# Kernel tuning notes

Hardware: AMD Instinct MI355X
Metric: run time of the kernel (lower is better)

Reference implementation:

```python
import jax, jax.numpy as jnp
import numpy as np

B, D, H, L, M = 32768, 768, 1024, 256, 32  # batch, input_dim, hidden, latent, context_memory_size
LN_EPS = 1e-5


def _ln(x, g, b):
    mu = jnp.mean(x, axis=-1, keepdims=True)
    var = jnp.mean(jnp.square(x - mu), axis=-1, keepdims=True)
    return (x - mu) * jax.lax.rsqrt(var + LN_EPS) * g + b


def _lrelu(x):
    return jnp.where(x >= 0, x, 0.2 * x)


def setup_inputs() -> dict:
    key = jax.random.key(0)
    ks = jax.random.split(key, 32)
    w = lambda k, shp: jax.random.normal(k, shp, jnp.float32) * (0.7 / np.sqrt(shp[-1]))
    return {
        "x": jax.random.normal(ks[0], (B, D), jnp.float32),
        "eps": jax.random.normal(ks[1], (B, L), jnp.float32),
        # encoder
        "enc_w1": w(ks[2], (H, D)), "enc_b1": jnp.zeros((H,), jnp.float32),
        "ln1_g": jnp.ones((H,), jnp.float32), "ln1_b": jnp.zeros((H,), jnp.float32),
        "enc_w2": w(ks[3], (H, H)), "enc_b2": jnp.zeros((H,), jnp.float32),
        "ln2_g": jnp.ones((H,), jnp.float32), "ln2_b": jnp.zeros((H,), jnp.float32),
        "mu_w": w(ks[4], (L, H)), "mu_b": jnp.zeros((L,), jnp.float32),
        "lv_w": w(ks[5], (L, H)), "lv_b": jnp.zeros((L,), jnp.float32),
        # decoder
        "di_w": w(ks[6], (H, L)), "di_b": jnp.zeros((H,), jnp.float32),
        "dec_w1": w(ks[7], (H, H)), "dec_b1": jnp.zeros((H,), jnp.float32),
        "dln1_g": jnp.ones((H,), jnp.float32), "dln1_b": jnp.zeros((H,), jnp.float32),
        "dec_w2": w(ks[8], (2 * H, H)), "dec_b2": jnp.zeros((2 * H,), jnp.float32),
        "dln2_g": jnp.ones((2 * H,), jnp.float32), "dln2_b": jnp.zeros((2 * H,), jnp.float32),
        "dec_w3": w(ks[9], (D, 2 * H)), "dec_b3": jnp.zeros((D,), jnp.float32),
        "ctx_mem": jax.random.normal(ks[10], (M, L), jnp.float32),
    }


def reference(x, eps, enc_w1, enc_b1, ln1_g, ln1_b, enc_w2, enc_b2, ln2_g, ln2_b,
              mu_w, mu_b, lv_w, lv_b, di_w, di_b, dec_w1, dec_b1, dln1_g, dln1_b,
              dec_w2, dec_b2, dln2_g, dln2_b, dec_w3, dec_b3, ctx_mem):
    # encode (Dropout is identity in eval mode)
    h = _lrelu(_ln(x @ enc_w1.T + enc_b1, ln1_g, ln1_b))
    h = _lrelu(_ln(h @ enc_w2.T + enc_b2, ln2_g, ln2_b))
    mu = h @ mu_w.T + mu_b
    logvar = h @ lv_w.T + lv_b
    # reparameterize
    z = mu + eps * jnp.exp(0.5 * logvar)
    # enhanced decode: context-memory attention
    attn = jax.nn.softmax(z @ ctx_mem.T, axis=-1)        # [B, M]
    z_enh = z + 0.1 * (attn @ ctx_mem)                   # [B, L]
    d = _lrelu(z_enh @ di_w.T + di_b)
    d = _lrelu(_ln(d @ dec_w1.T + dec_b1, dln1_g, dln1_b))
    d = _lrelu(_ln(d @ dec_w2.T + dec_b2, dln2_g, dln2_b))  # [B, 2H]
    reconstructed = d @ dec_w3.T + dec_b3                # [B, D]
    return reconstructed, mu, logvar
```

## Files before the change

### kernel.cpp

```cpp
#include <hip/hip_runtime.h>
#include <stdint.h>

#define DEV __device__ __forceinline__

typedef short bf16x8 __attribute__((ext_vector_type(8)));
typedef float f32x4 __attribute__((ext_vector_type(4)));

DEV ushort f2bf(float x) {
  uint32_t u = __builtin_bit_cast(uint32_t, x);
  return (ushort)((u + 0x7fffu + ((u >> 16) & 1u)) >> 16);
}
DEV float bf2f(ushort h) { return __builtin_bit_cast(float, (uint32_t)h << 16); }

DEV void gload_lds16(const void* g, void* l) {
  __builtin_amdgcn_global_load_lds((const __attribute__((address_space(1))) uint32_t*)g,
                                   (__attribute__((address_space(3))) uint32_t*)l, 16, 0, 0);
}

DEV bf16x8 ldv(const void* p) { return *(const bf16x8*)p; }

#define BARRIER __builtin_amdgcn_s_barrier()
#define SCHED0 __builtin_amdgcn_sched_barrier(0)
#define PRIO1 __builtin_amdgcn_s_setprio(1)
#define PRIO0 __builtin_amdgcn_s_setprio(0)
#define LGKM0                                        \
  do {                                               \
    asm volatile("s_waitcnt lgkmcnt(0)" ::: "memory"); \
    SCHED0;                                          \
  } while (0)

#define MFMA16(MH, NH, F, Bq)                                                   \
  _Pragma("unroll") for (int mi = 0; mi < 4; ++mi) {                            \
    _Pragma("unroll") for (int ni = 0; ni < 2; ++ni) {                          \
      acc[(MH)*4 + mi][(NH)*2 + ni] = __builtin_amdgcn_mfma_f32_16x16x32_bf16(  \
          F[mi][0], Bq[ni][0], acc[(MH)*4 + mi][(NH)*2 + ni], 0, 0, 0);         \
      acc[(MH)*4 + mi][(NH)*2 + ni] = __builtin_amdgcn_mfma_f32_16x16x32_bf16(  \
          F[mi][1], Bq[ni][1], acc[(MH)*4 + mi][(NH)*2 + ni], 0, 0, 0);         \
    }                                                                           \
  }

template <int EPI>
__global__ __launch_bounds__(512, 2) void g256(
    const ushort* __restrict__ A, int lda, const ushort* __restrict__ W, int ldb,
    void* __restrict__ Cv, long ldc, const float* __restrict__ bias,
    const float* __restrict__ bias2, long splitStride, int K) {
  __shared__ ushort As[2][256 * 64];
  __shared__ ushort Bs[2][256 * 64];
  const int t = threadIdx.x;
  const int l = t & 63;
  const int w = t >> 6;
  const int wm = w >> 2, wn = w & 3;

  const int nwg = gridDim.x * gridDim.y;
  int bid = blockIdx.y * gridDim.x + blockIdx.x;
  const int cpx = nwg >> 3;
  bid = (bid & 7) * cpx + (bid >> 3);
  const int bx = bid % gridDim.x;
  const int by = bid / gridDim.x;
  const long rowBase = (long)by << 8;
  const int colBase = bx << 8;

  const int srow = l >> 3;
  const int scol = ((l & 7) ^ srow) << 3;
  const ushort* aB = A + (size_t)(rowBase + srow) * lda + scol;
  const ushort* bB = W + (size_t)(colBase + srow) * ldb + scol;
  const int aC0 = wm * 16 + wn * 2;
  const int aC2 = aC0 + 8;
  const int bC0 = (wn >> 1) * 16 + (wm * 2 + (wn & 1)) * 4;

  const int fro = l & 15;
  const int o0 = (((l >> 4) << 4)) ^ ((l & 7) << 4);
  const int o1 = (64 + ((l >> 4) << 4)) ^ ((l & 7) << 4);

#define STG_A(KT1, CH) \
  gload_lds16(aB + (size_t)((CH) << 3) * lda + ((size_t)(KT1) << 6), \
              (char*)As[(KT1) & 1] + ((CH) << 10))
#define STG_B(KT1, CH) \
  gload_lds16(bB + (size_t)((CH) << 3) * ldb + ((size_t)(KT1) << 6), \
              (char*)Bs[(KT1) & 1] + ((CH) << 10))

  STG_A(0, aC0); STG_A(0, aC0 + 1);
  STG_B(0, bC0); STG_B(0, bC0 + 1); STG_B(0, bC0 + 2); STG_B(0, bC0 + 3);
  STG_A(0, aC2); STG_A(0, aC2 + 1);
  asm volatile("s_waitcnt vmcnt(2)" ::: "memory");
  BARRIER;

  const int nk = K >> 6;
  f32x4 acc[8][4] = {};
  bf16x8 af[4][2], b0[2][2], b1[2][2];

  for (int kt = 0; kt < nk; ++kt) {
    const int p = kt & 1;
    const bool stage = (kt + 1) < nk;
    const int kt1 = kt + 1;
    const char* Ap = (const char*)As[p] + (wm * 128 + fro) * 128;
    const char* Bp = (const char*)Bs[p] + (wn * 64 + fro) * 128;

#pragma unroll
    for (int mi = 0; mi < 4; ++mi) {
      af[mi][0] = ldv(Ap + mi * 2048 + o0);
      af[mi][1] = ldv(Ap + mi * 2048 + o1);
    }
#pragma unroll
    for (int ni = 0; ni < 2; ++ni) {
      b0[ni][0] = ldv(Bp + ni * 2048 + o0);
      b0[ni][1] = ldv(Bp + ni * 2048 + o1);
    }
    if (stage) { STG_A(kt1, aC0); STG_A(kt1, aC0 + 1); }
    BARRIER;
    LGKM0;
    PRIO1;
    MFMA16(0, 0, af, b0);
    SCHED0;
    PRIO0;
    BARRIER;

#pragma unroll
    for (int ni = 0; ni < 2; ++ni) {
      b1[ni][0] = ldv(Bp + 4096 + ni * 2048 + o0);
      b1[ni][1] = ldv(Bp + 4096 + ni * 2048 + o1);
    }
    if (stage) { STG_B(kt1, bC0); STG_B(kt1, bC0 + 1); }
    BARRIER;
    LGKM0;
    PRIO1;
    MFMA16(0, 1, af, b1);
    SCHED0;
    PRIO0;
    if (stage) asm volatile("s_waitcnt vmcnt(4)" ::: "memory");
    else       asm volatile("s_waitcnt vmcnt(0)" ::: "memory");
    BARRIER;

#pragma unroll
    for (int mi = 0; mi < 4; ++mi) {
      af[mi][0] = ldv(Ap + 8192 + mi * 2048 + o0);
      af[mi][1] = ldv(Ap + 8192 + mi * 2048 + o1);
    }
    if (stage) { STG_B(kt1, bC0 + 2); STG_B(kt1, bC0 + 3); }
    BARRIER;
    LGKM0;
    PRIO1;
    MFMA16(1, 1, af, b1);
    SCHED0;
    PRIO0;
    BARRIER;

    if (stage) { STG_A(kt1, aC2); STG_A(kt1, aC2 + 1); }
    BARRIER;
    SCHED0;
    PRIO1;
    MFMA16(1, 0, af, b0);
    SCHED0;
    PRIO0;
    if (stage) asm volatile("s_waitcnt vmcnt(2)" ::: "memory");
    BARRIER;
  }
#undef STG_A
#undef STG_B

  const int orow = (l >> 4) << 2;
  const int ocol = l & 15;
#pragma unroll
  for (int ni = 0; ni < 4; ++ni) {
    const int col = colBase + wn * 64 + ni * 16 + ocol;
    float bv;
    if (EPI == 3)
      bv = (col < 256) ? bias[col] : bias2[col - 256];
    else
      bv = bias[col];
#pragma unroll
    for (int mi = 0; mi < 8; ++mi) {
      const long row0 = rowBase + wm * 128 + mi * 16 + orow;
#pragma unroll
      for (int j = 0; j < 4; ++j) {
        float v = acc[mi][ni][j] + bv;
        if (EPI == 2) v = v >= 0.f ? v : 0.2f * v;
        if (EPI == 0) {
          ((float*)Cv)[(row0 + j) * ldc + col] = v;
        } else if (EPI == 3) {
          const long idx = (row0 + j) * 256 + (col & 255) + (long)(col >> 8) * splitStride;
          ((float*)Cv)[idx] = v;
        } else {
          ((ushort*)Cv)[(row0 + j) * ldc + col] = f2bf(v);
        }
      }
    }
  }
}

template <int N>
__global__ __launch_bounds__(256) void ln_lrelu(ushort* __restrict__ buf,
                                                const float* __restrict__ g,
                                                const float* __restrict__ b) {
  constexpr int E = N / 256;
  const int t = threadIdx.x;
  ushort* p = buf + (size_t)blockIdx.x * N + t * E;
  ushort us[E];
  *(ushort4*)&us[0] = *(const ushort4*)p;
  if constexpr (E == 8) *(ushort4*)&us[4] = *(const ushort4*)(p + 4);
  float f[E], s = 0.f, sq = 0.f;
#pragma unroll
  for (int j = 0; j < E; ++j) {
    f[j] = bf2f(us[j]);
    s += f[j];
    sq += f[j] * f[j];
  }
#pragma unroll
  for (int d = 32; d; d >>= 1) {
    s += __shfl_xor(s, d);
    sq += __shfl_xor(sq, d);
  }
  __shared__ float red[8];
  if ((t & 63) == 0) {
    red[(t >> 6) * 2] = s;
    red[(t >> 6) * 2 + 1] = sq;
  }
  __syncthreads();
  s = red[0] + red[2] + red[4] + red[6];
  sq = red[1] + red[3] + red[5] + red[7];
  const float mean = s * (1.f / N);
  const float rstd = rsqrtf(sq * (1.f / N) - mean * mean + 1e-5f);
  const float* gp = g + t * E;
  const float* bp = b + t * E;
#pragma unroll
  for (int j = 0; j < E; ++j) {
    float y = (f[j] - mean) * rstd * gp[j] + bp[j];
    y = y >= 0.f ? y : 0.2f * y;
    us[j] = f2bf(y);
  }
  *(ushort4*)p = *(ushort4*)&us[0];
  if constexpr (E == 8) *(ushort4*)(p + 4) = *(ushort4*)&us[4];
}

__global__ __launch_bounds__(256) void reparam_attn(
    const float* __restrict__ mu, const float* __restrict__ lv,
    const float* __restrict__ eps, const float* __restrict__ ctx,
    ushort* __restrict__ zb) {
  __shared__ float ctx_lds[32][257];
  __shared__ float z_lds[4][256];
  __shared__ float w_lds[4][32];
  const int t = threadIdx.x;
  for (int i = t; i < 32 * 256; i += 256) ctx_lds[i >> 8][i & 255] = ctx[i];
  __syncthreads();
  const int l = t & 63, wv = t >> 6;
  const int gw = blockIdx.x * 4 + wv;
  const int m = l & 31, half = l >> 5;
  for (int it = 0; it < 8; ++it) {
    const int r = gw + 4096 * it;
    const size_t base = (size_t)r * 256;
    float z[4];
#pragma unroll
    for (int j = 0; j < 4; ++j) {
      const int c = l + 64 * j;
      z[j] = mu[base + c] + eps[base + c] * __expf(0.5f * lv[base + c]);
      z_lds[wv][c] = z[j];
    }
    __syncthreads();
    float s = 0.f;
#pragma unroll 4
    for (int i2 = 0; i2 < 128; ++i2) {
      const int c = half * 128 + i2;
      s += ctx_lds[m][c] * z_lds[wv][c];
    }
    s += __shfl_xor(s, 32);
    float mx = s;
#pragma unroll
    for (int d2 = 16; d2; d2 >>= 1) mx = fmaxf(mx, __shfl_xor(mx, d2));
    const float e = __expf(s - mx);
    float sm = e;
#pragma unroll
    for (int d2 = 16; d2; d2 >>= 1) sm += __shfl_xor(sm, d2);
    w_lds[wv][m] = e / sm;
    __syncthreads();
#pragma unroll
    for (int j = 0; j < 4; ++j) {
      const int c = l + 64 * j;
      float a = 0.f;
#pragma unroll 8
      for (int mm = 0; mm < 32; ++mm) a += w_lds[wv][mm] * ctx_lds[mm][c];
      zb[base + c] = f2bf(z[j] + 0.1f * a);
    }
    __syncthreads();
  }
}

struct ConvArgs {
  const float* src[9];
  ushort* dst[9];
  int n4[9];
};
__global__ __launch_bounds__(256) void conv_bf16(ConvArgs a) {
  const int y = blockIdx.y;
  const float4* s = (const float4*)a.src[y];
  ushort4* d = (ushort4*)a.dst[y];
  const int n4 = a.n4[y];
  const int stride = gridDim.x * 256;
  for (int i = blockIdx.x * 256 + threadIdx.x; i < n4; i += stride) {
    float4 v = s[i];
    ushort4 o;
    o.x = f2bf(v.x); o.y = f2bf(v.y); o.z = f2bf(v.z); o.w = f2bf(v.w);
    d[i] = o;
  }
}

extern "C" void kernel_launch(void* const* d_in, const int* in_sizes, int n_in,
                              void* d_out, int out_size, void* d_ws, size_t ws_size,
                              hipStream_t stream) {
  constexpr size_t NB = 32768, ND = 768, NL = 256;

  const float* x = (const float*)d_in[0];
  const float* eps = (const float*)d_in[1];

  char* ws = (char*)d_ws;
  ushort* XB = (ushort*)(ws + 0);
  ushort* T1 = (ushort*)(ws + 0);
  ushort* T2 = (ushort*)(ws + 67108864ull);
  ushort* T3 = (ushort*)(ws + 67108864ull);
  ushort* ZB = (ushort*)(ws + 134217728ull);
  ushort* WB = (ushort*)(ws + 201326592ull);

  ushort* w1 = WB;
  ushort* w2 = w1 + 786432;
  ushort* wmu = w2 + 1048576;
  ushort* wlv = wmu + 262144;
  ushort* wdi = wlv + 262144;
  ushort* wd1 = wdi + 262144;
  ushort* wd2 = wd1 + 1048576;
  ushort* wd3 = wd2 + 2097152;

  ConvArgs ca;
  ca.src[0] = x;                      ca.dst[0] = XB;  ca.n4[0] = (int)(NB * ND / 4);
  ca.src[1] = (const float*)d_in[2];  ca.dst[1] = w1;  ca.n4[1] = 786432 / 4;
  ca.src[2] = (const float*)d_in[6];  ca.dst[2] = w2;  ca.n4[2] = 1048576 / 4;
  ca.src[3] = (const float*)d_in[10]; ca.dst[3] = wmu; ca.n4[3] = 262144 / 4;
  ca.src[4] = (const float*)d_in[12]; ca.dst[4] = wlv; ca.n4[4] = 262144 / 4;
  ca.src[5] = (const float*)d_in[14]; ca.dst[5] = wdi; ca.n4[5] = 262144 / 4;
  ca.src[6] = (const float*)d_in[16]; ca.dst[6] = wd1; ca.n4[6] = 1048576 / 4;
  ca.src[7] = (const float*)d_in[20]; ca.dst[7] = wd2; ca.n4[7] = 2097152 / 4;
  ca.src[8] = (const float*)d_in[24]; ca.dst[8] = wd3; ca.n4[8] = 1572864 / 4;
  conv_bf16<<<dim3(1024, 9), 256, 0, stream>>>(ca);

  float* out = (float*)d_out;
  float* mu_o = out + NB * ND;
  float* lv_o = mu_o + NB * NL;

  const long SPLIT = (long)NB * 256;

  g256<1><<<dim3(4, 128), 512, 0, stream>>>(XB, 768, w1, 768, T2, 1024,
                                            (const float*)d_in[3], nullptr, 0, 768);
  ln_lrelu<1024><<<32768, 256, 0, stream>>>(T2, (const float*)d_in[4], (const float*)d_in[5]);
  g256<1><<<dim3(4, 128), 512, 0, stream>>>(T2, 1024, w2, 1024, T1, 1024,
                                            (const float*)d_in[7], nullptr, 0, 1024);
  ln_lrelu<1024><<<32768, 256, 0, stream>>>(T1, (const float*)d_in[8], (const float*)d_in[9]);
  g256<3><<<dim3(2, 128), 512, 0, stream>>>(T1, 1024, wmu, 1024, mu_o, 256,
                                            (const float*)d_in[11], (const float*)d_in[13],
                                            SPLIT, 1024);
  reparam_attn<<<1024, 256, 0, stream>>>(mu_o, lv_o, eps, (const float*)d_in[26], ZB);
  g256<2><<<dim3(4, 128), 512, 0, stream>>>(ZB, 256, wdi, 256, T2, 1024,
                                            (const float*)d_in[15], nullptr, 0, 256);
  g256<1><<<dim3(4, 128), 512, 0, stream>>>(T2, 1024, wd1, 1024, T1, 1024,
                                            (const float*)d_in[17], nullptr, 0, 1024);
  ln_lrelu<1024><<<32768, 256, 0, stream>>>(T1, (const float*)d_in[18], (const float*)d_in[19]);
  g256<1><<<dim3(8, 128), 512, 0, stream>>>(T1, 1024, wd2, 1024, T3, 2048,
                                            (const float*)d_in[21], nullptr, 0, 1024);
  ln_lrelu<2048><<<32768, 256, 0, stream>>>(T3, (const float*)d_in[22], (const float*)d_in[23]);
  g256<0><<<dim3(3, 128), 512, 0, stream>>>(T3, 2048, wd3, 2048, out, 768,
                                            (const float*)d_in[25], nullptr, 0, 2048);
}
```

Measured before the change: 1.111 ms.

## Restage g256 pipeline by half-tiles and use simpler 128-tile GEMM for decoder

The 256x256 GEMM's shared-memory layout is reorganised into 128-row halves. Staging now prefetches A one k-step ahead and B two k-steps ahead, with wait counts and sched barriers adjusted to match. Two decoder GEMMs (latent-to-hidden and dec_w1) switch to a new single-buffered 128x128 tile kernel with 256 threads. The goal is deeper overlap of global loads with MFMA work in the main kernel. The risks are extra sync stalls in the simpler non-pipelined kernel and possible hazards in the reworked buffer reuse.

New measurement: 1.114 ms. Within noise of the previous version (+0.3%).

```diff
diff --git a/kernel.cpp b/kernel.cpp
--- a/kernel.cpp
+++ b/kernel.cpp
@@ -23,11 +23,12 @@
 #define SCHED0 __builtin_amdgcn_sched_barrier(0)
 #define PRIO1 __builtin_amdgcn_s_setprio(1)
 #define PRIO0 __builtin_amdgcn_s_setprio(0)
-#define LGKM0                                        \
-  do {                                               \
+#define LGKM0                                          \
+  do {                                                 \
     asm volatile("s_waitcnt lgkmcnt(0)" ::: "memory"); \
-    SCHED0;                                          \
+    SCHED0;                                            \
   } while (0)
+#define VMCNT(N) asm volatile("s_waitcnt vmcnt(" #N ")" ::: "memory")
 
 #define MFMA16(MH, NH, F, Bq)                                                   \
   _Pragma("unroll") for (int mi = 0; mi < 4; ++mi) {                            \
@@ -40,12 +41,95 @@
   }
 
 template <int EPI>
+__global__ __launch_bounds__(256, 2) void gemm_bt(
+    const ushort* __restrict__ A, int lda, const ushort* __restrict__ W, int ldb,
+    void* __restrict__ Cv, int ldc, const float* __restrict__ bias, int K) {
+  __shared__ ushort As[128 * 64];
+  __shared__ ushort Bs[128 * 64];
+  const int t = threadIdx.x;
+  const int l = t & 63;
+  const int w = t >> 6;
+  const int wr = w >> 1, wc = w & 1;
+  const int rowBase = blockIdx.y << 7;
+  const int colBase = blockIdx.x << 7;
+
+  const int cr = l >> 3;
+  const int ccol = ((l & 7) ^ cr) << 3;
+  const ushort* aS = A + (size_t)(rowBase + cr) * lda + ccol;
+  const ushort* bS = W + (size_t)(colBase + cr) * ldb + ccol;
+
+  f32x4 acc[4][4] = {};
+
+  const int nk = K >> 6;
+  for (int kt = 0; kt < nk; ++kt) {
+    if (kt) __syncthreads();
+    const int k0 = kt << 6;
+#pragma unroll
+    for (int c4 = 0; c4 < 4; ++c4) {
+      const int ch = (w << 2) + c4;
+      gload_lds16(aS + (size_t)(ch << 3) * lda + k0, (char*)As + (ch << 10));
+      gload_lds16(bS + (size_t)(ch << 3) * ldb + k0, (char*)Bs + (ch << 10));
+    }
+    __syncthreads();
+
+    bf16x8 af[2][4], bw[2][4];
+    const int koff = (l >> 4) << 4;
+#pragma unroll
+    for (int mi = 0; mi < 4; ++mi) {
+      const int r = (wr << 6) + (mi << 4) + (l & 15);
+      const char* rp = (const char*)As + (r << 7);
+      const int sw = (r & 7) << 4;
+      af[0][mi] = *(const bf16x8*)(rp + (koff ^ sw));
+      af[1][mi] = *(const bf16x8*)(rp + ((64 + koff) ^ sw));
+    }
+#pragma unroll
+    for (int ni = 0; ni < 4; ++ni) {
+      const int r = (wc << 6) + (ni << 4) + (l & 15);
+      const char* rp = (const char*)Bs + (r << 7);
+      const int sw = (r & 7) << 4;
+      bw[0][ni] = *(const bf16x8*)(rp + (koff ^ sw));
+      bw[1][ni] = *(const bf16x8*)(rp + ((64 + koff) ^ sw));
+    }
+#pragma unroll
+    for (int kk = 0; kk < 2; ++kk)
+#pragma unroll
+      for (int mi = 0; mi < 4; ++mi)
+#pragma unroll
+        for (int ni = 0; ni < 4; ++ni)
+          acc[mi][ni] = __builtin_amdgcn_mfma_f32_16x16x32_bf16(
+              af[kk][mi], bw[kk][ni], acc[mi][ni], 0, 0, 0);
+  }
+
+  const int orow = (l >> 4) << 2;
+  const int ocol = l & 15;
+#pragma unroll
+  for (int ni = 0; ni < 4; ++ni) {
+    const int col = colBase + (wc << 6) + (ni << 4) + ocol;
+    const float bv = bias[col];
+#pragma unroll
+    for (int mi = 0; mi < 4; ++mi) {
+      const int row0 = rowBase + (wr << 6) + (mi << 4) + orow;
+#pragma unroll
+      for (int j = 0; j < 4; ++j) {
+        float v = acc[mi][ni][j] + bv;
+        if (EPI == 2) v = v >= 0.f ? v : 0.2f * v;
+        const size_t idx = (size_t)(row0 + j) * ldc + col;
+        if (EPI == 0)
+          ((float*)Cv)[idx] = v;
+        else
+          ((ushort*)Cv)[idx] = f2bf(v);
+      }
+    }
+  }
+}
+
+template <int EPI>
 __global__ __launch_bounds__(512, 2) void g256(
     const ushort* __restrict__ A, int lda, const ushort* __restrict__ W, int ldb,
     void* __restrict__ Cv, long ldc, const float* __restrict__ bias,
     const float* __restrict__ bias2, long splitStride, int K) {
-  __shared__ ushort As[2][256 * 64];
-  __shared__ ushort Bs[2][256 * 64];
+  __shared__ ushort As[2 * 2 * 128 * 64];
+  __shared__ ushort Bs[2 * 2 * 128 * 64];
   const int t = threadIdx.x;
   const int l = t & 63;
   const int w = t >> 6;
@@ -62,39 +146,46 @@
 
   const int srow = l >> 3;
   const int scol = ((l & 7) ^ srow) << 3;
-  const ushort* aB = A + (size_t)(rowBase + srow) * lda + scol;
-  const ushort* bB = W + (size_t)(colBase + srow) * ldb + scol;
-  const int aC0 = wm * 16 + wn * 2;
-  const int aC2 = aC0 + 8;
-  const int bC0 = (wn >> 1) * 16 + (wm * 2 + (wn & 1)) * 4;
+  const ushort* aH[2] = {A + (size_t)(rowBase + srow) * lda + scol,
+                         A + (size_t)(rowBase + 128 + srow) * lda + scol};
+  const ushort* bH[2] = {W + (size_t)(colBase + srow) * ldb + scol,
+                         W + (size_t)(colBase + 128 + srow) * ldb + scol};
+
+#define STG_A(HALF, KTV, BUF)                                                \
+  _Pragma("unroll") for (int c = 0; c < 2; ++c) {                            \
+    const int ch = (w << 1) + c;                                             \
+    gload_lds16(aH[HALF] + (size_t)(ch << 3) * lda + ((size_t)(KTV) << 6),   \
+                (char*)As + ((BUF) << 15) + ((HALF) << 14) + (ch << 10));    \
+  }
+#define STG_B(HALF, KTV, BUF)                                                \
+  _Pragma("unroll") for (int c = 0; c < 2; ++c) {                            \
+    const int ch = (w << 1) + c;                                             \
+    gload_lds16(bH[HALF] + (size_t)(ch << 3) * ldb + ((size_t)(KTV) << 6),   \
+                (char*)Bs + ((BUF) << 15) + ((HALF) << 14) + (ch << 10));    \
+  }
 
   const int fro = l & 15;
-  const int o0 = (((l >> 4) << 4)) ^ ((l & 7) << 4);
-  const int o1 = (64 + ((l >> 4) << 4)) ^ ((l & 7) << 4);
-
-#define STG_A(KT1, CH) \
-  gload_lds16(aB + (size_t)((CH) << 3) * lda + ((size_t)(KT1) << 6), \
-              (char*)As[(KT1) & 1] + ((CH) << 10))
-#define STG_B(KT1, CH) \
-  gload_lds16(bB + (size_t)((CH) << 3) * ldb + ((size_t)(KT1) << 6), \
-              (char*)Bs[(KT1) & 1] + ((CH) << 10))
-
-  STG_A(0, aC0); STG_A(0, aC0 + 1);
-  STG_B(0, bC0); STG_B(0, bC0 + 1); STG_B(0, bC0 + 2); STG_B(0, bC0 + 3);
-  STG_A(0, aC2); STG_A(0, aC2 + 1);
-  asm volatile("s_waitcnt vmcnt(2)" ::: "memory");
+  const int koff = (l >> 4) << 4;
+  const int sw = (l & 7) << 4;
+  const int o0 = koff ^ sw;
+  const int o1 = (64 + koff) ^ sw;
+
+  const int nk = K >> 6;
+  STG_A(0, 0, 0); STG_A(1, 0, 0); STG_B(0, 0, 0); STG_B(1, 0, 0);
+  STG_B(0, 1, 1); STG_B(1, 1, 1);
+  VMCNT(4);
   BARRIER;
 
-  const int nk = K >> 6;
   f32x4 acc[8][4] = {};
   bf16x8 af[4][2], b0[2][2], b1[2][2];
 
   for (int kt = 0; kt < nk; ++kt) {
     const int p = kt & 1;
-    const bool stage = (kt + 1) < nk;
-    const int kt1 = kt + 1;
-    const char* Ap = (const char*)As[p] + (wm * 128 + fro) * 128;
-    const char* Bp = (const char*)Bs[p] + (wn * 64 + fro) * 128;
+    const bool sA = (kt + 1) < nk;
+    const bool sB = (kt + 2) < nk;
+    const char* Ap = (const char*)As + (p << 15) + (wm << 14) + fro * 128;
+    const char* Bp = (const char*)Bs + (p << 15) + ((wn >> 1) << 14) +
+                     ((wn & 1) << 13) + fro * 128;
 
 #pragma unroll
     for (int mi = 0; mi < 4; ++mi) {
@@ -106,12 +197,11 @@
       b0[ni][0] = ldv(Bp + ni * 2048 + o0);
       b0[ni][1] = ldv(Bp + ni * 2048 + o1);
     }
-    if (stage) { STG_A(kt1, aC0); STG_A(kt1, aC0 + 1); }
+    if (sA) STG_A(0, kt + 1, p ^ 1);
     BARRIER;
     LGKM0;
     PRIO1;
     MFMA16(0, 0, af, b0);
-    SCHED0;
     PRIO0;
     BARRIER;
 
@@ -120,15 +210,12 @@
       b1[ni][0] = ldv(Bp + 4096 + ni * 2048 + o0);
       b1[ni][1] = ldv(Bp + 4096 + ni * 2048 + o1);
     }
-    if (stage) { STG_B(kt1, bC0); STG_B(kt1, bC0 + 1); }
+    if (sA) STG_A(1, kt + 1, p ^ 1);
     BARRIER;
     LGKM0;
     PRIO1;
     MFMA16(0, 1, af, b1);
-    SCHED0;
     PRIO0;
-    if (stage) asm volatile("s_waitcnt vmcnt(4)" ::: "memory");
-    else       asm volatile("s_waitcnt vmcnt(0)" ::: "memory");
     BARRIER;
 
 #pragma unroll
@@ -136,23 +223,21 @@
       af[mi][0] = ldv(Ap + 8192 + mi * 2048 + o0);
       af[mi][1] = ldv(Ap + 8192 + mi * 2048 + o1);
     }
-    if (stage) { STG_B(kt1, bC0 + 2); STG_B(kt1, bC0 + 3); }
+    if (sB) STG_B(0, kt + 2, p);
     BARRIER;
     LGKM0;
     PRIO1;
     MFMA16(1, 1, af, b1);
-    SCHED0;
     PRIO0;
     BARRIER;
 
-    if (stage) { STG_A(kt1, aC2); STG_A(kt1, aC2 + 1); }
-    BARRIER;
-    SCHED0;
+    if (sB) STG_B(1, kt + 2, p);
+    BARRIER;
     PRIO1;
     MFMA16(1, 0, af, b0);
-    SCHED0;
     PRIO0;
-    if (stage) asm volatile("s_waitcnt vmcnt(2)" ::: "memory");
+    if (sB) VMCNT(4);
+    else if (sA) VMCNT(0);
     BARRIER;
   }
 #undef STG_A
@@ -356,10 +441,10 @@
                                             (const float*)d_in[11], (const float*)d_in[13],
                                             SPLIT, 1024);
   reparam_attn<<<1024, 256, 0, stream>>>(mu_o, lv_o, eps, (const float*)d_in[26], ZB);
-  g256<2><<<dim3(4, 128), 512, 0, stream>>>(ZB, 256, wdi, 256, T2, 1024,
-                                            (const float*)d_in[15], nullptr, 0, 256);
-  g256<1><<<dim3(4, 128), 512, 0, stream>>>(T2, 1024, wd1, 1024, T1, 1024,
-                                            (const float*)d_in[17], nullptr, 0, 1024);
+  gemm_bt<2><<<dim3(8, 256), 256, 0, stream>>>(ZB, 256, wdi, 256, T2, 1024,
+                                               (const float*)d_in[15], 256);
+  gemm_bt<1><<<dim3(8, 256), 256, 0, stream>>>(T2, 1024, wd1, 1024, T1, 1024,
+                                               (const float*)d_in[17], 1024);
   ln_lrelu<1024><<<32768, 256, 0, stream>>>(T1, (const float*)d_in[18], (const float*)d_in[19]);
   g256<1><<<dim3(8, 128), 512, 0, stream>>>(T1, 1024, wd2, 1024, T3, 2048,
                                             (const float*)d_in[21], nullptr, 0, 1024);
```
